# Optimization experiments

Hardware: AMD Instinct MI355X
Metric: run time of the kernel (lower is better)

The kernel has to match this reference:

```python
import jax, jax.numpy as jnp
import numpy as np

ITER_NUM = 3
BN_EPS = 1e-5
L2_EPS = 1e-12


def setup_inputs() -> dict:
    key = jax.random.key(0)
    k1, k2 = jax.random.split(key, 2)
    B, C, h, w = 64, 256, 14, 14
    E = 512
    feat = jax.random.normal(k1, (B, C, h, w), dtype=jnp.float32)
    W_proj = jax.random.normal(k2, (E, C * C), dtype=jnp.float32) * (1.0 / np.sqrt(C * C))
    b_proj = jnp.zeros((E,), dtype=jnp.float32)
    bn_gamma = jnp.ones((E,), dtype=jnp.float32)
    bn_beta = jnp.zeros((E,), dtype=jnp.float32)
    bn_mean = jnp.zeros((E,), dtype=jnp.float32)
    bn_var = jnp.ones((E,), dtype=jnp.float32)
    return {"feat": feat, "W_proj": W_proj, "b_proj": b_proj,
            "bn_gamma": bn_gamma, "bn_beta": bn_beta,
            "bn_mean": bn_mean, "bn_var": bn_var}


def _mpncov(feat):
    # feat: [B, C, h, w] -> [B, C, C] matrix square root of normalized covariance
    B, C, h, w = feat.shape
    M = h * w
    x = feat.reshape(B, C, M)
    # I_hat = I - (1/M) * ones  (centering matrix)
    I_hat = jnp.eye(M, dtype=feat.dtype) - (1.0 / M) * jnp.ones((M, M), dtype=feat.dtype)
    # y = x @ I_hat @ x^T / M  -> [B, C, C]
    xc = jnp.einsum('bcm,mn->bcn', x, I_hat)
    y = jnp.einsum('bcm,bdm->bcd', xc, x) / M
    trY = jnp.trace(y, axis1=-2, axis2=-1)  # [B]
    y = y / trY[:, None, None]
    I = jnp.broadcast_to(jnp.eye(C, dtype=feat.dtype), (B, C, C))
    Y, Z = y, I
    for _ in range(ITER_NUM):
        ZY = jnp.einsum('bij,bjk->bik', Z, Y)
        T = 3.0 * I - ZY
        Y = 0.5 * jnp.einsum('bij,bjk->bik', Y, T)
        Z = 0.5 * jnp.einsum('bij,bjk->bik', T, Z)
    return Y * jnp.sqrt(trY)[:, None, None]


def _l2_normalize(x, axis=-1):
    n = jnp.sqrt(jnp.sum(x * x, axis=axis, keepdims=True))
    return x / jnp.maximum(n, L2_EPS)


def reference(feat, W_proj, b_proj, bn_gamma, bn_beta, bn_mean, bn_var):
    B = feat.shape[0]
    pooled = _mpncov(feat)                      # [B, C, C]
    flat = pooled.reshape(B, -1)                # [B, C*C]
    flat = _l2_normalize(flat, axis=1)
    # dropout in eval mode = identity
    emb = flat @ W_proj.T + b_proj              # [B, E]
    # BatchNorm1d (inference mode, running stats)
    emb = (emb - bn_mean) * jax.lax.rsqrt(bn_var + BN_EPS) * bn_gamma + bn_beta
    norm_embedding = _l2_normalize(emb, axis=1)
    return norm_embedding
```

## Files before the change

kernel.cpp:

```cpp
#include <hip/hip_runtime.h>
#include <hip/hip_bf16.h>

#define BATCH 64
#define CDIM  256
#define MHW   196
#define MP    224
#define EDIM  512
#define CC    65536
#define NTRI  10
#define NMM   (BATCH * NTRI)

typedef __attribute__((ext_vector_type(8))) short short8_t;
typedef __attribute__((ext_vector_type(4))) float f32x4;
typedef __attribute__((ext_vector_type(4))) unsigned int u32x4;

static __device__ __forceinline__ short f2bf(float f) {
    __hip_bfloat16 h = __float2bfloat16(f);
    return (short)__builtin_bit_cast(unsigned short, h);
}

struct MMOp {
    const __hip_bfloat16* A;
    const __hip_bfloat16* B;
    const __hip_bfloat16* D;
    __hip_bfloat16*       out;
    const float*          alpha_ptr;
    int                   alpha_mode;
    float                 alpha_c, beta, gamma;
    float*                nrm;
};

__global__ __launch_bounds__(256) void k_center(const float* __restrict__ feat,
                                                __hip_bfloat16* __restrict__ xcb,
                                                float* __restrict__ rowsq)
{
    const int b  = blockIdx.x & 63;
    const int r4 = blockIdx.x >> 6;
    const int row = b * 256 + r4 * 4 + (threadIdx.x >> 6);
    const int l = threadIdx.x & 63;
    const float* src = feat + (size_t)row * MHW;
    float v0 = src[l];
    float v1 = src[l + 64];
    float v2 = src[l + 128];
    float v3 = (l + 192 < MHW) ? src[l + 192] : 0.0f;
    float s = v0 + v1 + v2 + v3;
    #pragma unroll
    for (int o = 32; o >= 1; o >>= 1) s += __shfl_xor(s, o, 64);
    const float mean = s * (1.0f / MHW);
    v0 -= mean; v1 -= mean; v2 -= mean;
    v3 = (l + 192 < MHW) ? (v3 - mean) : 0.0f;
    float sq = v0*v0 + v1*v1 + v2*v2 + v3*v3;
    #pragma unroll
    for (int o = 32; o >= 1; o >>= 1) sq += __shfl_xor(sq, o, 64);
    if (l == 0) rowsq[row] = sq;
    __hip_bfloat16* dst = xcb + (size_t)row * MP;
    dst[l]       = __float2bfloat16(v0);
    dst[l + 64]  = __float2bfloat16(v1);
    dst[l + 128] = __float2bfloat16(v2);
    if (l + 192 < MP) dst[l + 192] = __float2bfloat16(v3);
}

template<int KT, bool NORM>
__global__ __launch_bounds__(256) void k_mm(MMOp op0, MMOp op1)
{
    const MMOp op = (blockIdx.y == 0) ? op0 : op1;

    __shared__ __hip_bfloat16 As[64][72];
    __shared__ __hip_bfloat16 Bs[64][72];
    __shared__ float red[4];
    __shared__ float s_alpha;

    const int b = blockIdx.x & 63;
    const int t = blockIdx.x >> 6;
    int ti, tj;
    if (t < 4)      { ti = 0; tj = t; }
    else if (t < 7) { ti = 1; tj = t - 3; }
    else if (t < 9) { ti = 2; tj = t - 5; }
    else            { ti = 3; tj = 3; }

    const int tid = threadIdx.x;
    const int wv = tid >> 6, l = tid & 63;
    const int wr = wv >> 1, wc = wv & 1;
    const int lr = l & 15,  lg = l >> 4;

    if (op.alpha_mode) {
        float v = op.alpha_ptr[b * 256 + tid];
        #pragma unroll
        for (int o = 32; o >= 1; o >>= 1) v += __shfl_xor(v, o, 64);
        if (l == 0) red[wv] = v;
        __syncthreads();
        if (tid == 0) s_alpha = op.alpha_c / (red[0] + red[1] + red[2] + red[3]);
    } else if (tid == 0) {
        s_alpha = op.alpha_c;
    }

    const __hip_bfloat16* Ab = op.A + (size_t)b * (CDIM * KT) + (size_t)ti * 64 * KT;
    const __hip_bfloat16* Bb = op.B + (size_t)b * (CDIM * KT) + (size_t)tj * 64 * KT;

    f32x4 acc[2][2];
    #pragma unroll
    for (int i = 0; i < 2; i++)
        #pragma unroll
        for (int j = 0; j < 2; j++)
            #pragma unroll
            for (int r = 0; r < 4; r++) acc[i][j][r] = 0.0f;

    #pragma unroll
    for (int k0 = 0; k0 < KT; k0 += 64) {
        const int kw   = (KT - k0 >= 64) ? 64 : (KT - k0);
        const int segs = kw >> 3;
        __syncthreads();
        for (int u = tid; u < 64 * segs; u += 256) {
            const int row = u / segs;
            const int seg = u - row * segs;
            *reinterpret_cast<u32x4*>(&As[row][seg * 8]) =
                *reinterpret_cast<const u32x4*>(Ab + (size_t)row * KT + k0 + seg * 8);
            *reinterpret_cast<u32x4*>(&Bs[row][seg * 8]) =
                *reinterpret_cast<const u32x4*>(Bb + (size_t)row * KT + k0 + seg * 8);
        }
        __syncthreads();
        const int nks = kw >> 5;
        for (int ks = 0; ks < nks; ks++) {
            short8_t af[2], bfr[2];
            #pragma unroll
            for (int i = 0; i < 2; i++)
                af[i] = *reinterpret_cast<const short8_t*>(&As[wr * 32 + i * 16 + lr][ks * 32 + lg * 8]);
            #pragma unroll
            for (int j = 0; j < 2; j++)
                bfr[j] = *reinterpret_cast<const short8_t*>(&Bs[wc * 32 + j * 16 + lr][ks * 32 + lg * 8]);
            #pragma unroll
            for (int i = 0; i < 2; i++)
                #pragma unroll
                for (int j = 0; j < 2; j++)
                    acc[i][j] = __builtin_amdgcn_mfma_f32_16x16x32_bf16(af[i], bfr[j], acc[i][j], 0, 0, 0);
        }
    }

    const float a = s_alpha;
    __hip_bfloat16* ob = op.out + (size_t)b * CC;
    const __hip_bfloat16* Db = op.D ? (op.D + (size_t)b * CC) : nullptr;
    float ns = 0.0f;
    #pragma unroll
    for (int i = 0; i < 2; i++) {
        #pragma unroll
        for (int j = 0; j < 2; j++) {
            #pragma unroll
            for (int r = 0; r < 4; r++) {
                const int grow = ti * 64 + wr * 32 + i * 16 + lg * 4 + r;
                const int gcol = tj * 64 + wc * 32 + j * 16 + lr;
                float v = a * acc[i][j][r];
                if (Db) v += op.beta * __bfloat162float(Db[grow * 256 + gcol]);
                if (grow == gcol) v += op.gamma;
                const __hip_bfloat16 hv = __float2bfloat16(v);
                ob[grow * 256 + gcol] = hv;
                if (ti != tj) ob[gcol * 256 + grow] = hv;
                if (NORM) {
                    const float fv = __bfloat162float(hv);
                    ns += ((ti != tj) ? 2.0f : 1.0f) * fv * fv;
                }
            }
        }
    }
    if constexpr (NORM) {
        #pragma unroll
        for (int o = 32; o >= 1; o >>= 1) ns += __shfl_xor(ns, o, 64);
        __syncthreads();
        if (l == 0) red[wv] = ns;
        __syncthreads();
        if (tid == 0) op.nrm[b * NTRI + t] = red[0] + red[1] + red[2] + red[3];
    }
}

__global__ __launch_bounds__(256) void k_proj(const __hip_bfloat16* __restrict__ flat,
                                              const float* __restrict__ W,
                                              float* __restrict__ upart)
{
    __shared__ float racc[2][64][65];
    const int ks = blockIdx.x, et = blockIdx.y;
    const int tid = threadIdx.x, wv = tid >> 6, l = tid & 63;
    const int lr = l & 15, lg = l >> 4;
    const int kbase = ks * 1024 + wv * 256;

    f32x4 acc[4][4];
    #pragma unroll
    for (int i = 0; i < 4; i++)
        #pragma unroll
        for (int j = 0; j < 4; j++)
            #pragma unroll
            for (int r = 0; r < 4; r++) acc[i][j][r] = 0.0f;

    for (int kk = 0; kk < 256; kk += 32) {
        const int k = kbase + kk + lg * 8;
        short8_t af[4];
        #pragma unroll
        for (int i = 0; i < 4; i++)
            af[i] = *reinterpret_cast<const short8_t*>(flat + (size_t)(i * 16 + lr) * CC + k);
        short8_t bfr[4];
        #pragma unroll
        for (int j = 0; j < 4; j++) {
            const f32x4* wp = reinterpret_cast<const f32x4*>(W + (size_t)(et * 64 + j * 16 + lr) * CC + k);
            const f32x4 w0 = wp[0], w1 = wp[1];
            short8_t s;
            s[0] = f2bf(w0[0]); s[1] = f2bf(w0[1]); s[2] = f2bf(w0[2]); s[3] = f2bf(w0[3]);
            s[4] = f2bf(w1[0]); s[5] = f2bf(w1[1]); s[6] = f2bf(w1[2]); s[7] = f2bf(w1[3]);
            bfr[j] = s;
        }
        #pragma unroll
        for (int i = 0; i < 4; i++)
            #pragma unroll
            for (int j = 0; j < 4; j++)
                acc[i][j] = __builtin_amdgcn_mfma_f32_16x16x32_bf16(af[i], bfr[j], acc[i][j], 0, 0, 0);
    }

    if (wv >= 2) {
        #pragma unroll
        for (int i = 0; i < 4; i++)
            #pragma unroll
            for (int j = 0; j < 4; j++)
                #pragma unroll
                for (int r = 0; r < 4; r++)
                    racc[wv - 2][i * 16 + lg * 4 + r][j * 16 + lr] = acc[i][j][r];
    }
    __syncthreads();
    if (wv < 2) {
        #pragma unroll
        for (int i = 0; i < 4; i++)
            #pragma unroll
            for (int j = 0; j < 4; j++)
                #pragma unroll
                for (int r = 0; r < 4; r++)
                    racc[wv][i * 16 + lg * 4 + r][j * 16 + lr] += acc[i][j][r];
    }
    __syncthreads();
    float* ub = upart + (size_t)ks * (64 * EDIM);
    #pragma unroll
    for (int q = 0; q < 16; q++) {
        const int idx = q * 256 + tid;
        const int x = idx >> 6, y = idx & 63;
        ub[(size_t)x * EDIM + et * 64 + y] = racc[0][x][y] + racc[1][x][y];
    }
}

__global__ __launch_bounds__(256) void k_fin(const float* __restrict__ upart,
                                             const float* __restrict__ nrmp,
                                             const float* __restrict__ bias,
                                             const float* __restrict__ gma,
                                             const float* __restrict__ bta,
                                             const float* __restrict__ mu,
                                             const float* __restrict__ var,
                                             float* __restrict__ out)
{
    __shared__ float wsum[4];
    const int bb = blockIdx.x;
    const int tid = threadIdx.x, wv = tid >> 6, l = tid & 63;
    const int e0 = tid, e1 = tid + 256;
    float u0 = 0.0f, u1 = 0.0f;
    for (int p = 0; p < 64; ++p) {
        const float* up = upart + ((size_t)p * 64 + bb) * EDIM;
        u0 += up[e0]; u1 += up[e1];
    }
    float fro = 0.0f;
    #pragma unroll
    for (int q = 0; q < NTRI; ++q) fro += nrmp[bb * NTRI + q];
    const float s = 1.0f / fmaxf(sqrtf(fro), 1e-12f);
    const float emb0 = s * u0 + bias[e0];
    const float emb1 = s * u1 + bias[e1];
    const float v0 = (emb0 - mu[e0]) * rsqrtf(var[e0] + 1e-5f) * gma[e0] + bta[e0];
    const float v1 = (emb1 - mu[e1]) * rsqrtf(var[e1] + 1e-5f) * gma[e1] + bta[e1];
    float sq = v0 * v0 + v1 * v1;
    #pragma unroll
    for (int o = 32; o >= 1; o >>= 1) sq += __shfl_xor(sq, o, 64);
    if (l == 0) wsum[wv] = sq;
    __syncthreads();
    const float tot = wsum[0] + wsum[1] + wsum[2] + wsum[3];
    const float rn = 1.0f / fmaxf(sqrtf(tot), 1e-12f);
    out[(size_t)bb * EDIM + e0] = v0 * rn;
    out[(size_t)bb * EDIM + e1] = v1 * rn;
}

extern "C" void kernel_launch(void* const* d_in, const int* in_sizes, int n_in,
                              void* d_out, int out_size, void* d_ws, size_t ws_size,
                              hipStream_t stream)
{
    const float* feat = (const float*)d_in[0];
    const float* W    = (const float*)d_in[1];
    const float* bias = (const float*)d_in[2];
    const float* gma  = (const float*)d_in[3];
    const float* bta  = (const float*)d_in[4];
    const float* mu   = (const float*)d_in[5];
    const float* var  = (const float*)d_in[6];
    float* out = (float*)d_out;

    char* ws = (char*)d_ws;
    constexpr size_t XCB_BYTES = (size_t)BATCH * CDIM * MP * 2;
    constexpr size_t MATB      = (size_t)BATCH * CC * 2;
    constexpr size_t OFF_ROWSQ = 4096;
    constexpr size_t OFF_XCB   = OFF_ROWSQ + (size_t)BATCH * CDIM * 4;
    constexpr size_t OFF_M     = OFF_XCB + XCB_BYTES;
    constexpr size_t OFF_UP    = OFF_M + 5 * MATB;
    constexpr size_t NEEDED    = OFF_UP + (size_t)64 * 64 * EDIM * 4;
    if (ws_size < NEEDED) return;

    float* nrmp  = (float*)(ws + 1024);
    float* rowsq = (float*)(ws + OFF_ROWSQ);
    __hip_bfloat16* xcb = (__hip_bfloat16*)(ws + OFF_XCB);
    __hip_bfloat16* M0  = (__hip_bfloat16*)(ws + OFF_M + 0 * MATB);
    __hip_bfloat16* M1  = (__hip_bfloat16*)(ws + OFF_M + 1 * MATB);
    __hip_bfloat16* M2  = (__hip_bfloat16*)(ws + OFF_M + 2 * MATB);
    __hip_bfloat16* M3  = (__hip_bfloat16*)(ws + OFF_M + 3 * MATB);
    __hip_bfloat16* M4  = (__hip_bfloat16*)(ws + OFF_M + 4 * MATB);
    float* upart = (float*)(ws + OFF_UP);

    k_center<<<dim3(4096), 256, 0, stream>>>(feat, xcb, rowsq);

    const dim3 g1(NMM, 1), g2(NMM, 2), blk(256);
    MMOp nop = {};

    MMOp cov = {xcb, xcb, nullptr, M0, rowsq, 1, 1.0f, 0.0f, 0.0f, nullptr};
    k_mm<MP, false><<<g1, blk, 0, stream>>>(cov, nop);
    MMOp y1 = {M0, M0, M0, M1, nullptr, 0, -0.5f, 1.5f, 0.0f, nullptr};
    k_mm<256, false><<<g1, blk, 0, stream>>>(y1, nop);
    MMOp t2 = {M0, M1, M1, M2, nullptr, 0, 0.5f, -1.5f, 3.0f, nullptr};
    k_mm<256, false><<<g1, blk, 0, stream>>>(t2, nop);
    MMOp y2 = {M1, M2, nullptr, M3, nullptr, 0, 0.5f, 0.0f, 0.0f, nullptr};
    MMOp z2 = {M2, M0, M2, M4, nullptr, 0, -0.25f, 0.75f, 0.0f, nullptr};
    k_mm<256, false><<<g2, blk, 0, stream>>>(y2, z2);
    MMOp t3 = {M4, M3, nullptr, M1, nullptr, 0, -1.0f, 0.0f, 3.0f, nullptr};
    k_mm<256, false><<<g1, blk, 0, stream>>>(t3, nop);
    MMOp y3 = {M3, M1, nullptr, M2, nullptr, 0, 0.5f, 0.0f, 0.0f, nrmp};
    k_mm<256, true ><<<g1, blk, 0, stream>>>(y3, nop);

    k_proj<<<dim3(64, 8), blk, 0, stream>>>(M2, W, upart);
    k_fin<<<dim3(64), blk, 0, stream>>>(upart, nrmp, bias, gma, bta, mu, var, out);
}
```

Measured before the change: 115.1 us.

## Split-K across wave pairs in k_mm and read A directly from global

```diff
diff --git a/kernel.cpp b/kernel.cpp
--- a/kernel.cpp
+++ b/kernel.cpp
@@ -61,13 +61,15 @@
 }
 
 template<int KT, bool NORM>
-__global__ __launch_bounds__(256) void k_mm(MMOp op0, MMOp op1)
-{
+__global__ __launch_bounds__(512, 4) void k_mm(MMOp op0, MMOp op1)
+{
+    constexpr int KH0  = 128;
+    constexpr int SEGS = KT / 8;
     const MMOp op = (blockIdx.y == 0) ? op0 : op1;
 
-    __shared__ __hip_bfloat16 As[64][72];
-    __shared__ __hip_bfloat16 Bs[64][72];
+    __shared__ __hip_bfloat16 Bs[64][264];
     __shared__ float red[4];
+    __shared__ float red2[4];
     __shared__ float s_alpha;
 
     const int b = blockIdx.x & 63;
@@ -79,24 +81,35 @@
     else            { ti = 3; tj = 3; }
 
     const int tid = threadIdx.x;
-    const int wv = tid >> 6, l = tid & 63;
-    const int wr = wv >> 1, wc = wv & 1;
+    const int w = tid >> 6, l = tid & 63;
+    const int kh = w & 1, sp = w >> 1;
+    const int si = sp >> 1, sj = sp & 1;
     const int lr = l & 15,  lg = l >> 4;
 
     if (op.alpha_mode) {
-        float v = op.alpha_ptr[b * 256 + tid];
-        #pragma unroll
-        for (int o = 32; o >= 1; o >>= 1) v += __shfl_xor(v, o, 64);
-        if (l == 0) red[wv] = v;
+        if (tid < 256) {
+            float v = op.alpha_ptr[b * 256 + tid];
+            #pragma unroll
+            for (int o = 32; o >= 1; o >>= 1) v += __shfl_xor(v, o, 64);
+            if (l == 0) red[tid >> 6] = v;
+        }
         __syncthreads();
         if (tid == 0) s_alpha = op.alpha_c / (red[0] + red[1] + red[2] + red[3]);
     } else if (tid == 0) {
         s_alpha = op.alpha_c;
     }
 
-    const __hip_bfloat16* Ab = op.A + (size_t)b * (CDIM * KT) + (size_t)ti * 64 * KT;
     const __hip_bfloat16* Bb = op.B + (size_t)b * (CDIM * KT) + (size_t)tj * 64 * KT;
-
+    for (int u = tid; u < 64 * SEGS; u += 512) {
+        const int row = u / SEGS;
+        const int seg = u - row * SEGS;
+        *reinterpret_cast<u32x4*>(&Bs[row][seg * 8]) =
+            *reinterpret_cast<const u32x4*>(Bb + (size_t)row * KT + seg * 8);
+    }
+    __syncthreads();
+
+    const __hip_bfloat16* Ab = op.A + (size_t)b * (CDIM * KT)
+                             + (size_t)(ti * 64 + si * 32) * KT;
     f32x4 acc[2][2];
     #pragma unroll
     for (int i = 0; i < 2; i++)
@@ -105,69 +118,87 @@
             #pragma unroll
             for (int r = 0; r < 4; r++) acc[i][j][r] = 0.0f;
 
-    #pragma unroll
-    for (int k0 = 0; k0 < KT; k0 += 64) {
-        const int kw   = (KT - k0 >= 64) ? 64 : (KT - k0);
-        const int segs = kw >> 3;
-        __syncthreads();
-        for (int u = tid; u < 64 * segs; u += 256) {
-            const int row = u / segs;
-            const int seg = u - row * segs;
-            *reinterpret_cast<u32x4*>(&As[row][seg * 8]) =
-                *reinterpret_cast<const u32x4*>(Ab + (size_t)row * KT + k0 + seg * 8);
-            *reinterpret_cast<u32x4*>(&Bs[row][seg * 8]) =
-                *reinterpret_cast<const u32x4*>(Bb + (size_t)row * KT + k0 + seg * 8);
-        }
-        __syncthreads();
-        const int nks = kw >> 5;
-        for (int ks = 0; ks < nks; ks++) {
-            short8_t af[2], bfr[2];
-            #pragma unroll
-            for (int i = 0; i < 2; i++)
-                af[i] = *reinterpret_cast<const short8_t*>(&As[wr * 32 + i * 16 + lr][ks * 32 + lg * 8]);
+#define MM_BODY(K0)                                                              \
+    {                                                                            \
+        const int k = (K0) + lg * 8;                                             \
+        short8_t af[2], bfr[2];                                                  \
+        _Pragma("unroll")                                                        \
+        for (int i = 0; i < 2; i++)                                              \
+            af[i] = *reinterpret_cast<const short8_t*>(                          \
+                        Ab + (size_t)(i * 16 + lr) * KT + k);                    \
+        _Pragma("unroll")                                                        \
+        for (int j = 0; j < 2; j++)                                              \
+            bfr[j] = *reinterpret_cast<const short8_t*>(                         \
+                         &Bs[sj * 32 + j * 16 + lr][k]);                         \
+        _Pragma("unroll")                                                        \
+        for (int i = 0; i < 2; i++)                                              \
+            _Pragma("unroll")                                                    \
+            for (int j = 0; j < 2; j++)                                          \
+                acc[i][j] = __builtin_amdgcn_mfma_f32_16x16x32_bf16(             \
+                                af[i], bfr[j], acc[i][j], 0, 0, 0);              \
+    }
+
+    if (kh == 0) {
+        #pragma unroll
+        for (int k0 = 0; k0 < KH0; k0 += 32) MM_BODY(k0);
+    } else {
+        #pragma unroll
+        for (int k0 = KH0; k0 < KT; k0 += 32) MM_BODY(k0);
+    }
+#undef MM_BODY
+
+    __syncthreads();
+    float* racc = reinterpret_cast<float*>(Bs);
+
+    if (kh == 0) {
+        #pragma unroll
+        for (int i = 0; i < 2; i++)
             #pragma unroll
             for (int j = 0; j < 2; j++)
-                bfr[j] = *reinterpret_cast<const short8_t*>(&Bs[wc * 32 + j * 16 + lr][ks * 32 + lg * 8]);
-            #pragma unroll
-            for (int i = 0; i < 2; i++)
                 #pragma unroll
-                for (int j = 0; j < 2; j++)
-                    acc[i][j] = __builtin_amdgcn_mfma_f32_16x16x32_bf16(af[i], bfr[j], acc[i][j], 0, 0, 0);
-        }
-    }
-
-    const float a = s_alpha;
-    __hip_bfloat16* ob = op.out + (size_t)b * CC;
-    const __hip_bfloat16* Db = op.D ? (op.D + (size_t)b * CC) : nullptr;
+                for (int r = 0; r < 4; r++)
+                    racc[(sp * 32 + i * 16 + lg * 4 + r) * 33 + j * 16 + lr] =
+                        acc[i][j][r];
+    }
+    __syncthreads();
+
     float ns = 0.0f;
-    #pragma unroll
-    for (int i = 0; i < 2; i++) {
-        #pragma unroll
-        for (int j = 0; j < 2; j++) {
-            #pragma unroll
-            for (int r = 0; r < 4; r++) {
-                const int grow = ti * 64 + wr * 32 + i * 16 + lg * 4 + r;
-                const int gcol = tj * 64 + wc * 32 + j * 16 + lr;
-                float v = a * acc[i][j][r];
-                if (Db) v += op.beta * __bfloat162float(Db[grow * 256 + gcol]);
-                if (grow == gcol) v += op.gamma;
-                const __hip_bfloat16 hv = __float2bfloat16(v);
-                ob[grow * 256 + gcol] = hv;
-                if (ti != tj) ob[gcol * 256 + grow] = hv;
-                if (NORM) {
-                    const float fv = __bfloat162float(hv);
-                    ns += ((ti != tj) ? 2.0f : 1.0f) * fv * fv;
+    if (kh == 1) {
+        const float a = s_alpha;
+        __hip_bfloat16* ob = op.out + (size_t)b * CC;
+        const __hip_bfloat16* Db = op.D ? (op.D + (size_t)b * CC) : nullptr;
+        #pragma unroll
+        for (int i = 0; i < 2; i++) {
+            #pragma unroll
+            for (int j = 0; j < 2; j++) {
+                #pragma unroll
+                for (int r = 0; r < 4; r++) {
+                    const int lrow = i * 16 + lg * 4 + r;
+                    const int lcol = j * 16 + lr;
+                    const int grow = ti * 64 + si * 32 + lrow;
+                    const int gcol = tj * 64 + sj * 32 + lcol;
+                    float v = a * (acc[i][j][r] + racc[(sp * 32 + lrow) * 33 + lcol]);
+                    if (Db) v += op.beta * __bfloat162float(Db[grow * 256 + gcol]);
+                    if (grow == gcol) v += op.gamma;
+                    const __hip_bfloat16 hv = __float2bfloat16(v);
+                    ob[grow * 256 + gcol] = hv;
+                    if (ti != tj) ob[gcol * 256 + grow] = hv;
+                    if (NORM) {
+                        const float fv = __bfloat162float(hv);
+                        ns += ((ti != tj) ? 2.0f : 1.0f) * fv * fv;
+                    }
                 }
             }
         }
+        if (NORM) {
+            #pragma unroll
+            for (int o = 32; o >= 1; o >>= 1) ns += __shfl_xor(ns, o, 64);
+            if (l == 0) red2[sp] = ns;
+        }
     }
     if constexpr (NORM) {
-        #pragma unroll
-        for (int o = 32; o >= 1; o >>= 1) ns += __shfl_xor(ns, o, 64);
         __syncthreads();
-        if (l == 0) red[wv] = ns;
-        __syncthreads();
-        if (tid == 0) op.nrm[b * NTRI + t] = red[0] + red[1] + red[2] + red[3];
+        if (tid == 0) op.nrm[b * NTRI + t] = red2[0] + red2[1] + red2[2] + red2[3];
     }
 }
 
@@ -313,7 +344,7 @@
 
     k_center<<<dim3(4096), 256, 0, stream>>>(feat, xcb, rowsq);
 
-    const dim3 g1(NMM, 1), g2(NMM, 2), blk(256);
+    const dim3 g1(NMM, 1), g2(NMM, 2), blk(512);
     MMOp nop = {};
 
     MMOp cov = {xcb, xcb, nullptr, M0, rowsq, 1, 1.0f, 0.0f, 0.0f, nullptr};
@@ -330,6 +361,6 @@
     MMOp y3 = {M3, M1, nullptr, M2, nullptr, 0, 0.5f, 0.0f, 0.0f, nrmp};
     k_mm<256, true ><<<g1, blk, 0, stream>>>(y3, nop);
 
-    k_proj<<<dim3(64, 8), blk, 0, stream>>>(M2, W, upart);
-    k_fin<<<dim3(64), blk, 0, stream>>>(upart, nrmp, bias, gma, bta, mu, var, out);
-}
+    k_proj<<<dim3(64, 8), dim3(256), 0, stream>>>(M2, W, upart);
+    k_fin<<<dim3(64), dim3(256), 0, stream>>>(upart, nrmp, bias, gma, bta, mu, var, out);
+}
```

New measurement: 139.2 us. 20.9% more time.

## Fuse centering into covariance kernel and defer trace normalization to later GEMMs

Applied to the files above, without the earlier changes.

```diff
diff --git a/kernel.cpp b/kernel.cpp
--- a/kernel.cpp
+++ b/kernel.cpp
@@ -24,21 +24,17 @@
     const __hip_bfloat16* B;
     const __hip_bfloat16* D;
     __hip_bfloat16*       out;
-    const float*          alpha_ptr;
-    int                   alpha_mode;
+    const float*          trp;
+    int                   apow;
+    int                   bpow;
     float                 alpha_c, beta, gamma;
     float*                nrm;
 };
 
-__global__ __launch_bounds__(256) void k_center(const float* __restrict__ feat,
-                                                __hip_bfloat16* __restrict__ xcb,
-                                                float* __restrict__ rowsq)
-{
-    const int b  = blockIdx.x & 63;
-    const int r4 = blockIdx.x >> 6;
-    const int row = b * 256 + r4 * 4 + (threadIdx.x >> 6);
-    const int l = threadIdx.x & 63;
-    const float* src = feat + (size_t)row * MHW;
+static __device__ __forceinline__ float center_to_lds(
+    const float* __restrict__ fb, int row, __hip_bfloat16* __restrict__ dst, int l)
+{
+    const float* src = fb + (size_t)row * MHW;
     float v0 = src[l];
     float v1 = src[l + 64];
     float v2 = src[l + 128];
@@ -52,23 +48,20 @@
     float sq = v0*v0 + v1*v1 + v2*v2 + v3*v3;
     #pragma unroll
     for (int o = 32; o >= 1; o >>= 1) sq += __shfl_xor(sq, o, 64);
-    if (l == 0) rowsq[row] = sq;
-    __hip_bfloat16* dst = xcb + (size_t)row * MP;
     dst[l]       = __float2bfloat16(v0);
     dst[l + 64]  = __float2bfloat16(v1);
     dst[l + 128] = __float2bfloat16(v2);
     if (l + 192 < MP) dst[l + 192] = __float2bfloat16(v3);
-}
-
-template<int KT, bool NORM>
-__global__ __launch_bounds__(256) void k_mm(MMOp op0, MMOp op1)
-{
-    const MMOp op = (blockIdx.y == 0) ? op0 : op1;
-
-    __shared__ __hip_bfloat16 As[64][72];
-    __shared__ __hip_bfloat16 Bs[64][72];
+    return sq;
+}
+
+__global__ __launch_bounds__(256) void k_cov(const float* __restrict__ feat,
+                                             __hip_bfloat16* __restrict__ Cout,
+                                             float* __restrict__ trpart)
+{
+    __shared__ __hip_bfloat16 As[64][232];
+    __shared__ __hip_bfloat16 Bs[64][232];
     __shared__ float red[4];
-    __shared__ float s_alpha;
 
     const int b = blockIdx.x & 63;
     const int t = blockIdx.x >> 6;
@@ -82,16 +75,102 @@
     const int wv = tid >> 6, l = tid & 63;
     const int wr = wv >> 1, wc = wv & 1;
     const int lr = l & 15,  lg = l >> 4;
-
-    if (op.alpha_mode) {
-        float v = op.alpha_ptr[b * 256 + tid];
-        #pragma unroll
-        for (int o = 32; o >= 1; o >>= 1) v += __shfl_xor(v, o, 64);
-        if (l == 0) red[wv] = v;
-        __syncthreads();
-        if (tid == 0) s_alpha = op.alpha_c / (red[0] + red[1] + red[2] + red[3]);
-    } else if (tid == 0) {
-        s_alpha = op.alpha_c;
+    const float* fb = feat + (size_t)b * (CDIM * MHW);
+
+    float sqacc = 0.0f;
+    #pragma unroll 2
+    for (int r = 0; r < 16; ++r) {
+        const int lrow = wv * 16 + r;
+        sqacc += center_to_lds(fb, ti * 64 + lrow, &As[lrow][0], l);
+    }
+    if (ti != tj) {
+        #pragma unroll 2
+        for (int r = 0; r < 16; ++r) {
+            const int lrow = wv * 16 + r;
+            center_to_lds(fb, tj * 64 + lrow, &Bs[lrow][0], l);
+        }
+    }
+    if (l == 0) red[wv] = sqacc;
+    __syncthreads();
+    if (ti == tj && tid == 0)
+        trpart[b * 4 + ti] = red[0] + red[1] + red[2] + red[3];
+
+    const __hip_bfloat16 (*Bp)[232] = (ti == tj) ? As : Bs;
+
+    f32x4 acc[2][2];
+    #pragma unroll
+    for (int i = 0; i < 2; i++)
+        #pragma unroll
+        for (int j = 0; j < 2; j++)
+            #pragma unroll
+            for (int r = 0; r < 4; r++) acc[i][j][r] = 0.0f;
+
+    #pragma unroll
+    for (int ks = 0; ks < MP / 32; ks++) {
+        short8_t af[2], bfr[2];
+        #pragma unroll
+        for (int i = 0; i < 2; i++)
+            af[i] = *reinterpret_cast<const short8_t*>(&As[wr * 32 + i * 16 + lr][ks * 32 + lg * 8]);
+        #pragma unroll
+        for (int j = 0; j < 2; j++)
+            bfr[j] = *reinterpret_cast<const short8_t*>(&Bp[wc * 32 + j * 16 + lr][ks * 32 + lg * 8]);
+        #pragma unroll
+        for (int i = 0; i < 2; i++)
+            #pragma unroll
+            for (int j = 0; j < 2; j++)
+                acc[i][j] = __builtin_amdgcn_mfma_f32_16x16x32_bf16(af[i], bfr[j], acc[i][j], 0, 0, 0);
+    }
+
+    __hip_bfloat16* ob = Cout + (size_t)b * CC;
+    #pragma unroll
+    for (int i = 0; i < 2; i++)
+        #pragma unroll
+        for (int j = 0; j < 2; j++)
+            #pragma unroll
+            for (int r = 0; r < 4; r++) {
+                const int grow = ti * 64 + wr * 32 + i * 16 + lg * 4 + r;
+                const int gcol = tj * 64 + wc * 32 + j * 16 + lr;
+                const __hip_bfloat16 hv = __float2bfloat16(acc[i][j][r]);
+                ob[grow * 256 + gcol] = hv;
+                if (ti != tj) ob[gcol * 256 + grow] = hv;
+            }
+}
+
+template<bool NORM>
+__global__ __launch_bounds__(256) void k_mm(MMOp op0, MMOp op1)
+{
+    constexpr int KT = 256;
+    const MMOp op = (blockIdx.y == 0) ? op0 : op1;
+
+    __shared__ __hip_bfloat16 As[64][72];
+    __shared__ __hip_bfloat16 Bs[64][72];
+    __shared__ float red[4];
+    __shared__ float s_alpha;
+    __shared__ float s_beta;
+
+    const int b = blockIdx.x & 63;
+    const int t = blockIdx.x >> 6;
+    int ti, tj;
+    if (t < 4)      { ti = 0; tj = t; }
+    else if (t < 7) { ti = 1; tj = t - 3; }
+    else if (t < 9) { ti = 2; tj = t - 5; }
+    else            { ti = 3; tj = 3; }
+
+    const int tid = threadIdx.x;
+    const int wv = tid >> 6, l = tid & 63;
+    const int wr = wv >> 1, wc = wv & 1;
+    const int lr = l & 15,  lg = l >> 4;
+
+    if (tid == 0) {
+        float sa = op.alpha_c, sb = op.beta;
+        if (op.apow | op.bpow) {
+            const float* tp = op.trp + b * 4;
+            const float itr = 1.0f / (tp[0] + tp[1] + tp[2] + tp[3]);
+            if (op.apow) sa *= (op.apow == 2) ? itr * itr : itr;
+            if (op.bpow) sb *= itr;
+        }
+        s_alpha = sa;
+        s_beta  = sb;
     }
 
     const __hip_bfloat16* Ab = op.A + (size_t)b * (CDIM * KT) + (size_t)ti * 64 * KT;
@@ -107,20 +186,18 @@
 
     #pragma unroll
     for (int k0 = 0; k0 < KT; k0 += 64) {
-        const int kw   = (KT - k0 >= 64) ? 64 : (KT - k0);
-        const int segs = kw >> 3;
         __syncthreads();
-        for (int u = tid; u < 64 * segs; u += 256) {
-            const int row = u / segs;
-            const int seg = u - row * segs;
+        for (int u = tid; u < 64 * 8; u += 256) {
+            const int row = u >> 3;
+            const int seg = u & 7;
             *reinterpret_cast<u32x4*>(&As[row][seg * 8]) =
                 *reinterpret_cast<const u32x4*>(Ab + (size_t)row * KT + k0 + seg * 8);
             *reinterpret_cast<u32x4*>(&Bs[row][seg * 8]) =
                 *reinterpret_cast<const u32x4*>(Bb + (size_t)row * KT + k0 + seg * 8);
         }
         __syncthreads();
-        const int nks = kw >> 5;
-        for (int ks = 0; ks < nks; ks++) {
+        #pragma unroll
+        for (int ks = 0; ks < 2; ks++) {
             short8_t af[2], bfr[2];
             #pragma unroll
             for (int i = 0; i < 2; i++)
@@ -136,7 +213,8 @@
         }
     }
 
-    const float a = s_alpha;
+    const float a  = s_alpha;
+    const float sb = s_beta;
     __hip_bfloat16* ob = op.out + (size_t)b * CC;
     const __hip_bfloat16* Db = op.D ? (op.D + (size_t)b * CC) : nullptr;
     float ns = 0.0f;
@@ -149,7 +227,7 @@
                 const int grow = ti * 64 + wr * 32 + i * 16 + lg * 4 + r;
                 const int gcol = tj * 64 + wc * 32 + j * 16 + lr;
                 float v = a * acc[i][j][r];
-                if (Db) v += op.beta * __bfloat162float(Db[grow * 256 + gcol]);
+                if (Db) v += sb * __bfloat162float(Db[grow * 256 + gcol]);
                 if (grow == gcol) v += op.gamma;
                 const __hip_bfloat16 hv = __float2bfloat16(v);
                 ob[grow * 256 + gcol] = hv;
@@ -292,43 +370,36 @@
     float* out = (float*)d_out;
 
     char* ws = (char*)d_ws;
-    constexpr size_t XCB_BYTES = (size_t)BATCH * CDIM * MP * 2;
-    constexpr size_t MATB      = (size_t)BATCH * CC * 2;
-    constexpr size_t OFF_ROWSQ = 4096;
-    constexpr size_t OFF_XCB   = OFF_ROWSQ + (size_t)BATCH * CDIM * 4;
-    constexpr size_t OFF_M     = OFF_XCB + XCB_BYTES;
-    constexpr size_t OFF_UP    = OFF_M + 5 * MATB;
-    constexpr size_t NEEDED    = OFF_UP + (size_t)64 * 64 * EDIM * 4;
+    constexpr size_t MATB   = (size_t)BATCH * CC * 2;
+    constexpr size_t OFF_M  = 8192;
+    constexpr size_t OFF_UP = OFF_M + 5 * MATB;
+    constexpr size_t NEEDED = OFF_UP + (size_t)64 * 64 * EDIM * 4;
     if (ws_size < NEEDED) return;
 
-    float* nrmp  = (float*)(ws + 1024);
-    float* rowsq = (float*)(ws + OFF_ROWSQ);
-    __hip_bfloat16* xcb = (__hip_bfloat16*)(ws + OFF_XCB);
-    __hip_bfloat16* M0  = (__hip_bfloat16*)(ws + OFF_M + 0 * MATB);
-    __hip_bfloat16* M1  = (__hip_bfloat16*)(ws + OFF_M + 1 * MATB);
-    __hip_bfloat16* M2  = (__hip_bfloat16*)(ws + OFF_M + 2 * MATB);
-    __hip_bfloat16* M3  = (__hip_bfloat16*)(ws + OFF_M + 3 * MATB);
-    __hip_bfloat16* M4  = (__hip_bfloat16*)(ws + OFF_M + 4 * MATB);
+    float* nrmp   = (float*)(ws + 1024);
+    float* trpart = (float*)(ws + 4096);
+    __hip_bfloat16* M0 = (__hip_bfloat16*)(ws + OFF_M + 0 * MATB);
+    __hip_bfloat16* M1 = (__hip_bfloat16*)(ws + OFF_M + 1 * MATB);
+    __hip_bfloat16* M2 = (__hip_bfloat16*)(ws + OFF_M + 2 * MATB);
+    __hip_bfloat16* M3 = (__hip_bfloat16*)(ws + OFF_M + 3 * MATB);
+    __hip_bfloat16* M4 = (__hip_bfloat16*)(ws + OFF_M + 4 * MATB);
     float* upart = (float*)(ws + OFF_UP);
-
-    k_center<<<dim3(4096), 256, 0, stream>>>(feat, xcb, rowsq);
 
     const dim3 g1(NMM, 1), g2(NMM, 2), blk(256);
     MMOp nop = {};
 
-    MMOp cov = {xcb, xcb, nullptr, M0, rowsq, 1, 1.0f, 0.0f, 0.0f, nullptr};
-    k_mm<MP, false><<<g1, blk, 0, stream>>>(cov, nop);
-    MMOp y1 = {M0, M0, M0, M1, nullptr, 0, -0.5f, 1.5f, 0.0f, nullptr};
-    k_mm<256, false><<<g1, blk, 0, stream>>>(y1, nop);
-    MMOp t2 = {M0, M1, M1, M2, nullptr, 0, 0.5f, -1.5f, 3.0f, nullptr};
-    k_mm<256, false><<<g1, blk, 0, stream>>>(t2, nop);
-    MMOp y2 = {M1, M2, nullptr, M3, nullptr, 0, 0.5f, 0.0f, 0.0f, nullptr};
-    MMOp z2 = {M2, M0, M2, M4, nullptr, 0, -0.25f, 0.75f, 0.0f, nullptr};
-    k_mm<256, false><<<g2, blk, 0, stream>>>(y2, z2);
-    MMOp t3 = {M4, M3, nullptr, M1, nullptr, 0, -1.0f, 0.0f, 3.0f, nullptr};
-    k_mm<256, false><<<g1, blk, 0, stream>>>(t3, nop);
-    MMOp y3 = {M3, M1, nullptr, M2, nullptr, 0, 0.5f, 0.0f, 0.0f, nrmp};
-    k_mm<256, true ><<<g1, blk, 0, stream>>>(y3, nop);
+    k_cov<<<g1, blk, 0, stream>>>(feat, M0, trpart);
+    MMOp y1 = {M0, M0, M0, M1, trpart, 2, 1, -0.5f, 1.5f, 0.0f, nullptr};
+    k_mm<false><<<g1, blk, 0, stream>>>(y1, nop);
+    MMOp t2 = {M0, M1, M1, M2, trpart, 1, 0, 0.5f, -1.5f, 3.0f, nullptr};
+    k_mm<false><<<g1, blk, 0, stream>>>(t2, nop);
+    MMOp y2 = {M1, M2, nullptr, M3, nullptr, 0, 0, 0.5f, 0.0f, 0.0f, nullptr};
+    MMOp z2 = {M2, M0, M2, M4, trpart, 1, 0, -0.25f, 0.75f, 0.0f, nullptr};
+    k_mm<false><<<g2, blk, 0, stream>>>(y2, z2);
+    MMOp t3 = {M4, M3, nullptr, M1, nullptr, 0, 0, -1.0f, 0.0f, 3.0f, nullptr};
+    k_mm<false><<<g1, blk, 0, stream>>>(t3, nop);
+    MMOp y3 = {M3, M1, nullptr, M2, nullptr, 0, 0, 0.5f, 0.0f, 0.0f, nrmp};
+    k_mm<true ><<<g1, blk, 0, stream>>>(y3, nop);
 
     k_proj<<<dim3(64, 8), blk, 0, stream>>>(M2, W, upart);
     k_fin<<<dim3(64), blk, 0, stream>>>(upart, nrmp, bias, gma, bta, mu, var, out);
```

New measurement: 131.7 us. 1.14x slower.
